# Optimization experiments

Measured on AMD Instinct MI355X. Metric: run time of the kernel, lower is better.

The kernel has to match this reference:

```python
import jax, jax.numpy as jnp
import numpy as np

SR = 16000
N_WT = 10
WT_LEN = 512
FIR_TAPS = 31
NU_C = 0.1
N_REFLECT = (FIR_TAPS - 1) // 2
B, L = 16, 160000


def setup_inputs() -> dict:
    key = jax.random.key(0)
    k1, k2, k3, k4 = jax.random.split(key, 4)
    # F0 in a realistic [100, 400) Hz range
    pitch = jax.random.uniform(k1, (B, L, 1), jnp.float32) * 300.0 + 100.0
    envelope = jax.random.uniform(k2, (B, L, 1), jnp.float32)
    # attention weights are 'already softmaxed' over the wavetable axis
    attention = jax.nn.softmax(jax.random.normal(k3, (B, L, N_WT), jnp.float32), axis=-1)
    # learned wavetables, init N(0, 0.01) as in the torch module (n_pure_harmonics=0)
    wavetables = jax.random.normal(k4, (N_WT, WT_LEN), jnp.float32) * 0.01
    # fixed windowed-sinc low-pass FIR (Type I), same construction as __init__
    n = np.arange(-(FIR_TAPS - 1) // 2, 1 + (FIR_TAPS - 1) // 2, dtype=np.float32)
    h = 2.0 * NU_C * np.sinc(2.0 * NU_C * n) * np.hamming(FIR_TAPS)
    fir_h = jnp.asarray(h, jnp.float32)
    return {"pitch": pitch, "envelope": envelope, "attention": attention,
            "wavetables": wavetables, "fir_h": fir_h}


def reference(pitch, envelope, attention, wavetables, fir_h):
    # circular ('reflect' in the repo's naming) pad each wavetable: (W, 512+2*15)
    wt_pad = jnp.concatenate(
        [wavetables[:, -N_REFLECT:], wavetables, wavetables[:, :N_REFLECT]], axis=1)
    # torch conv1d is cross-correlation; jnp.correlate 'valid' matches -> (W, 512)
    wt = jax.vmap(lambda x: jnp.correlate(x, fir_h, mode='valid'))(wt_pad)

    L_wt = WT_LEN
    freqs = pitch[..., 0]                       # (B, L)
    increment = (L_wt / SR) * freqs             # phase increment per sample
    # NOTE: faithful to torch code: increment[0] is the FIRST BATCH ROW (L,)
    index = jnp.cumsum(increment, axis=1) - increment[0]
    index = jnp.remainder(index, L_wt)
    index = jnp.where(L_wt - index < 1e-5, 0.0, index)
    idx_lo_f = jnp.floor(index)
    alpha = index - idx_lo_f                    # (B, L)
    i_lo = idx_lo_f.astype(jnp.int32)
    i_hi = jnp.ceil(index).astype(jnp.int32) % L_wt

    # gather all wavetables at once: (W, B, L)
    lo = jnp.take(wt, i_lo, axis=1)
    hi = jnp.take(wt, i_hi, axis=1)
    wave = lo + alpha[None, :, :] * (hi - lo)   # linear interpolation
    wave = jnp.transpose(wave, (1, 2, 0))       # (B, L, W)

    out = jnp.sum(wave * attention, axis=2, keepdims=True) * envelope  # (B, L, 1)
    return out
```

## Files before the change

### kernel.cpp

```cpp
#include <hip/hip_runtime.h>

#define N_WT_     10
#define WT_LEN_   512
#define FIR_TAPS_ 31
#define N_REFL_   15
#define B_        16
#define L_        160000

constexpr int   TPB   = 256;
constexpr float INCF  = 0.032f;
constexpr int   NG0   = L_ / 16;
constexpr int   NG1   = NG0 / 16;
constexpr int   NG2   = 40;
constexpr int   NG3   = 3;
constexpr int   CPB   = 5;
constexpr int   WTI   = (WT_LEN_ + 1) * N_WT_;

__global__ void fir_kernel(const float* __restrict__ wavetables,
                           const float* __restrict__ fir_h,
                           float* __restrict__ wt2) {
    __shared__ float s_pad[WT_LEN_ + 2 * N_REFL_];
    __shared__ float s_h[FIR_TAPS_];
    const int w = blockIdx.x;
    const int i = threadIdx.x;
    if (i < FIR_TAPS_) s_h[i] = fir_h[i];
    for (int j = i; j < WT_LEN_ + 2 * N_REFL_; j += blockDim.x) {
        int src = (j + WT_LEN_ - N_REFL_) % WT_LEN_;
        s_pad[j] = wavetables[w * WT_LEN_ + src];
    }
    __syncthreads();
    float acc = 0.0f;
#pragma unroll
    for (int t = 0; t < FIR_TAPS_; ++t)
        acc = fmaf(s_h[t], s_pad[i + t], acc);
    wt2[i * N_WT_ + w] = acc;
    if (i == 0) wt2[WT_LEN_ * N_WT_ + w] = acc;
}

__global__ __launch_bounds__(TPB) void ysum_kernel(
        const float* __restrict__ pitch, float* __restrict__ y) {
    __shared__ float s_x[4096];
    const int b = blockIdx.y, bx = blockIdx.x, t = threadIdx.x;
    const float* prow = pitch + (size_t)b * L_;
    const int x0 = bx * 4096;
    for (int i = t; i < 4096; i += TPB) {
        int l = x0 + i;
        s_x[i] = (l < L_) ? INCF * prow[l] : 0.0f;
    }
    __syncthreads();
    const int g = bx * 256 + t;
    if (g < NG0) {
        const float* p = s_x + (g * 16 - x0);
        float acc = 0.0f;
        for (int i = 0; i < 16; ++i) acc += p[i];
        y[b * NG0 + g] = acc;
    }
}

__global__ __launch_bounds__(TPB) void scan_kernel(
        const float* __restrict__ y, float* __restrict__ S1) {
    __shared__ float s_y[NG0];
    __shared__ float s_S1[NG0];
    __shared__ float s_z[NG1];
    __shared__ float s_S2[NG1];
    __shared__ float s_w[NG2], s_S3[NG2];
    __shared__ float s_v[NG3], s_S4[NG3];
    const int b = blockIdx.x, t = threadIdx.x;
    const float* yrow = y + (size_t)b * NG0;
    for (int i = t; i < NG0; i += TPB) s_y[i] = yrow[i];
    __syncthreads();
    for (int j = t; j < NG1; j += TPB) {
        float a = 0.0f;
        for (int i = 0; i < 16; ++i) a += s_y[16 * j + i];
        s_z[j] = a;
    }
    __syncthreads();
    if (t < NG2) {
        float a = 0.0f;
        int hi = min(16 * t + 16, NG1);
        for (int i = 16 * t; i < hi; ++i) a += s_z[i];
        s_w[t] = a;
    }
    __syncthreads();
    if (t < NG3) {
        float a = 0.0f;
        int hi = min(16 * t + 16, NG2);
        for (int i = 16 * t; i < hi; ++i) a += s_w[i];
        s_v[t] = a;
    }
    __syncthreads();
    if (t == 0) {
        float run = 0.0f;
        for (int m = 0; m < NG3; ++m) { run += s_v[m]; s_S4[m] = run; }
    }
    __syncthreads();
    if (t < NG2) {
        float a = 0.0f;
        for (int i = (t >> 4) << 4; i <= t; ++i) a += s_w[i];
        if (t >= 16) a = a + s_S4[(t >> 4) - 1];
        s_S3[t] = a;
    }
    __syncthreads();
    if (t < NG2) {
        float r = 0.0f;
        float carry = (t > 0) ? s_S3[t - 1] : 0.0f;
        int hi = min(16 * t + 16, NG1);
        for (int k = 16 * t; k < hi; ++k) {
            r += s_z[k];
            s_S2[k] = (t > 0) ? r + carry : r;
        }
    }
    __syncthreads();
    for (int j = t; j < NG1; j += TPB) {
        float r = 0.0f;
        float carry = (j > 0) ? s_S2[j - 1] : 0.0f;
        for (int k = 0; k < 16; ++k) {
            r += s_y[16 * j + k];
            s_S1[16 * j + k] = (j > 0) ? r + carry : r;
        }
    }
    __syncthreads();
    float* S1row = S1 + (size_t)b * NG0;
    for (int i = t; i < NG0; i += TPB) S1row[i] = s_S1[i];
}

__global__ __launch_bounds__(TPB) void synth_kernel(
        const float* __restrict__ pitch,
        const float* __restrict__ envelope,
        const float* __restrict__ attention,
        const float* __restrict__ wt2,
        const float* __restrict__ S1,
        float* __restrict__ out) {
    __shared__ float s_wt[WTI];
    const int b = blockIdx.y, cb = blockIdx.x, t = threadIdx.x;
    for (int i = t; i < WTI; i += TPB) s_wt[i] = wt2[i];
    __syncthreads();

    const int lane = t & 63;
    const int r16  = lane & 15;
    const int sbase = lane & ~15;
    const size_t rowb = (size_t)b * L_;
    const float* S1row = S1 + (size_t)b * NG0;

    for (int cc = 0; cc < CPB; ++cc) {
        const int    l = (cb * CPB + cc) * TPB + t;
        const size_t g = rowb + l;

        float x = INCF * pitch[g];
        float acc = 0.0f;
#pragma unroll
        for (int k = 0; k < 16; ++k) {
            float v = __shfl(x, sbase + k, 64);
            acc += (k <= r16) ? v : 0.0f;
        }
        const int g0 = l >> 4;
        if (g0 > 0) acc = acc + S1row[g0 - 1];

        float idx = acc - INCF * pitch[l];
        float r = fmodf(idx, 512.0f);
        if (r < 0.0f) r += 512.0f;
        if (512.0f - r < 1e-5f) r = 0.0f;
        float fl = floorf(r);
        float alpha = r - fl;
        int lo = (int)fl;

        const float2* pw = (const float2*)(s_wt + lo * N_WT_);
        float2 q0 = pw[0], q1 = pw[1], q2 = pw[2], q3 = pw[3], q4 = pw[4];
        float2 q5 = pw[5], q6 = pw[6], q7 = pw[7], q8 = pw[8], q9 = pw[9];
        float loV[10] = {q0.x, q0.y, q1.x, q1.y, q2.x, q2.y, q3.x, q3.y, q4.x, q4.y};
        float hiV[10] = {q5.x, q5.y, q6.x, q6.y, q7.x, q7.y, q8.x, q8.y, q9.x, q9.y};

        const float2* ap = (const float2*)(attention + g * N_WT_);
        float2 a01 = ap[0], a23 = ap[1], a45 = ap[2], a67 = ap[3], a89 = ap[4];
        float a[10] = {a01.x, a01.y, a23.x, a23.y, a45.x, a45.y,
                       a67.x, a67.y, a89.x, a89.y};

        float a0 = 0.0f;
#pragma unroll
        for (int w = 0; w < N_WT_; ++w)
            a0 += a[w] * (loV[w] + alpha * (hiV[w] - loV[w]));
        out[g] = a0 * envelope[g];
    }
}

extern "C" void kernel_launch(void* const* d_in, const int* in_sizes, int n_in,
                              void* d_out, int out_size, void* d_ws, size_t ws_size,
                              hipStream_t stream) {
    const float* pitch      = (const float*)d_in[0];
    const float* envelope   = (const float*)d_in[1];
    const float* attention  = (const float*)d_in[2];
    const float* wavetables = (const float*)d_in[3];
    const float* fir_h      = (const float*)d_in[4];
    float*       out        = (float*)d_out;

    char*  ws  = (char*)d_ws;
    float* wt2 = (float*)(ws);
    float* y   = (float*)(ws + 32768);
    float* S1  = (float*)(ws + 32768 + 655360);

    fir_kernel<<<dim3(N_WT_), dim3(WT_LEN_), 0, stream>>>(wavetables, fir_h, wt2);
    ysum_kernel<<<dim3(40, B_), dim3(TPB), 0, stream>>>(pitch, y);
    scan_kernel<<<dim3(B_), dim3(TPB), 0, stream>>>(y, S1);
    synth_kernel<<<dim3(L_ / (TPB * CPB), B_), dim3(TPB), 0, stream>>>(
        pitch, envelope, attention, wt2, S1, out);
}
```

Baseline: 203.2 us.

## Fuse FIR into ysum, widen scan block, one chunk per synth block

The FIR wavetable filter moves into the first ten blocks of the ysum kernel, which removes one kernel launch. The scan kernel runs with 1024 threads and copies rows with float2 loads and stores. The synth kernel now handles one 256-element chunk per block and has many more blocks. Its global loads (pitch, envelope, attention, carry) are issued before the shared wavetable fill so they overlap it. In exchange, each synth block reloads the whole shared wavetable for less work, and the fused blocks carry extra FIR work and shared memory.

```diff
diff --git a/kernel.cpp b/kernel.cpp
--- a/kernel.cpp
+++ b/kernel.cpp
@@ -8,39 +8,32 @@
 #define L_        160000
 
 constexpr int   TPB   = 256;
+constexpr int   TPS   = 1024;
 constexpr float INCF  = 0.032f;
 constexpr int   NG0   = L_ / 16;
 constexpr int   NG1   = NG0 / 16;
 constexpr int   NG2   = 40;
 constexpr int   NG3   = 3;
-constexpr int   CPB   = 5;
 constexpr int   WTI   = (WT_LEN_ + 1) * N_WT_;
 
-__global__ void fir_kernel(const float* __restrict__ wavetables,
-                           const float* __restrict__ fir_h,
-                           float* __restrict__ wt2) {
+__global__ __launch_bounds__(TPB) void ysum_kernel(
+        const float* __restrict__ pitch, float* __restrict__ y,
+        const float* __restrict__ wavetables, const float* __restrict__ fir_h,
+        float* __restrict__ wt2) {
+    __shared__ float s_x[4096];
     __shared__ float s_pad[WT_LEN_ + 2 * N_REFL_];
     __shared__ float s_h[FIR_TAPS_];
-    const int w = blockIdx.x;
-    const int i = threadIdx.x;
-    if (i < FIR_TAPS_) s_h[i] = fir_h[i];
-    for (int j = i; j < WT_LEN_ + 2 * N_REFL_; j += blockDim.x) {
-        int src = (j + WT_LEN_ - N_REFL_) % WT_LEN_;
-        s_pad[j] = wavetables[w * WT_LEN_ + src];
-    }
-    __syncthreads();
-    float acc = 0.0f;
-#pragma unroll
-    for (int t = 0; t < FIR_TAPS_; ++t)
-        acc = fmaf(s_h[t], s_pad[i + t], acc);
-    wt2[i * N_WT_ + w] = acc;
-    if (i == 0) wt2[WT_LEN_ * N_WT_ + w] = acc;
-}
-
-__global__ __launch_bounds__(TPB) void ysum_kernel(
-        const float* __restrict__ pitch, float* __restrict__ y) {
-    __shared__ float s_x[4096];
     const int b = blockIdx.y, bx = blockIdx.x, t = threadIdx.x;
+
+    const bool do_fir = (b == 0) && (bx < N_WT_);
+    if (do_fir) {
+        if (t < FIR_TAPS_) s_h[t] = fir_h[t];
+        for (int j = t; j < WT_LEN_ + 2 * N_REFL_; j += TPB) {
+            int src = (j + WT_LEN_ - N_REFL_) % WT_LEN_;
+            s_pad[j] = wavetables[bx * WT_LEN_ + src];
+        }
+    }
+
     const float* prow = pitch + (size_t)b * L_;
     const int x0 = bx * 4096;
     for (int i = t; i < 4096; i += TPB) {
@@ -48,6 +41,18 @@
         s_x[i] = (l < L_) ? INCF * prow[l] : 0.0f;
     }
     __syncthreads();
+
+    if (do_fir) {
+        for (int i = t; i < WT_LEN_; i += TPB) {
+            float acc = 0.0f;
+#pragma unroll
+            for (int tap = 0; tap < FIR_TAPS_; ++tap)
+                acc = fmaf(s_h[tap], s_pad[i + tap], acc);
+            wt2[i * N_WT_ + bx] = acc;
+            if (i == 0) wt2[WT_LEN_ * N_WT_ + bx] = acc;
+        }
+    }
+
     const int g = bx * 256 + t;
     if (g < NG0) {
         const float* p = s_x + (g * 16 - x0);
@@ -57,19 +62,23 @@
     }
 }
 
-__global__ __launch_bounds__(TPB) void scan_kernel(
+__global__ __launch_bounds__(TPS) void scan_kernel(
         const float* __restrict__ y, float* __restrict__ S1) {
-    __shared__ float s_y[NG0];
-    __shared__ float s_S1[NG0];
+    __shared__ __align__(16) float s_y[NG0];
+    __shared__ __align__(16) float s_S1[NG0];
     __shared__ float s_z[NG1];
     __shared__ float s_S2[NG1];
     __shared__ float s_w[NG2], s_S3[NG2];
     __shared__ float s_v[NG3], s_S4[NG3];
     const int b = blockIdx.x, t = threadIdx.x;
     const float* yrow = y + (size_t)b * NG0;
-    for (int i = t; i < NG0; i += TPB) s_y[i] = yrow[i];
-    __syncthreads();
-    for (int j = t; j < NG1; j += TPB) {
+    {
+        const float2* src = (const float2*)yrow;
+        float2* dst = (float2*)s_y;
+        for (int i = t; i < NG0 / 2; i += TPS) dst[i] = src[i];
+    }
+    __syncthreads();
+    for (int j = t; j < NG1; j += TPS) {
         float a = 0.0f;
         for (int i = 0; i < 16; ++i) a += s_y[16 * j + i];
         s_z[j] = a;
@@ -111,7 +120,7 @@
         }
     }
     __syncthreads();
-    for (int j = t; j < NG1; j += TPB) {
+    for (int j = t; j < NG1; j += TPS) {
         float r = 0.0f;
         float carry = (j > 0) ? s_S2[j - 1] : 0.0f;
         for (int k = 0; k < 16; ++k) {
@@ -121,7 +130,11 @@
     }
     __syncthreads();
     float* S1row = S1 + (size_t)b * NG0;
-    for (int i = t; i < NG0; i += TPB) S1row[i] = s_S1[i];
+    {
+        const float2* src = (const float2*)s_S1;
+        float2* dst = (float2*)S1row;
+        for (int i = t; i < NG0 / 2; i += TPS) dst[i] = src[i];
+    }
 }
 
 __global__ __launch_bounds__(TPB) void synth_kernel(
@@ -131,56 +144,60 @@
         const float* __restrict__ wt2,
         const float* __restrict__ S1,
         float* __restrict__ out) {
-    __shared__ float s_wt[WTI];
+    __shared__ __align__(16) float s_wt[WTI];
     const int b = blockIdx.y, cb = blockIdx.x, t = threadIdx.x;
-    for (int i = t; i < WTI; i += TPB) s_wt[i] = wt2[i];
-    __syncthreads();
-
-    const int lane = t & 63;
-    const int r16  = lane & 15;
+    const int    l = cb * TPB + t;
+    const size_t g = (size_t)b * L_ + l;
+
+    const float pv  = pitch[g];
+    const float p0  = pitch[l];
+    const float env = envelope[g];
+    const int   g0  = l >> 4;
+    const float carry = (g0 > 0) ? S1[(size_t)b * NG0 + g0 - 1] : 0.0f;
+    const float2* ap = (const float2*)(attention + g * (size_t)N_WT_);
+    float2 a01 = ap[0], a23 = ap[1], a45 = ap[2], a67 = ap[3], a89 = ap[4];
+
+    {
+        const float2* src = (const float2*)wt2;
+        float2* dst = (float2*)s_wt;
+        for (int i = t; i < WTI / 2; i += TPB) dst[i] = src[i];
+    }
+    __syncthreads();
+
+    const int lane  = t & 63;
+    const int r16   = lane & 15;
     const int sbase = lane & ~15;
-    const size_t rowb = (size_t)b * L_;
-    const float* S1row = S1 + (size_t)b * NG0;
-
-    for (int cc = 0; cc < CPB; ++cc) {
-        const int    l = (cb * CPB + cc) * TPB + t;
-        const size_t g = rowb + l;
-
-        float x = INCF * pitch[g];
-        float acc = 0.0f;
+
+    float x = INCF * pv;
+    float acc = 0.0f;
 #pragma unroll
-        for (int k = 0; k < 16; ++k) {
-            float v = __shfl(x, sbase + k, 64);
-            acc += (k <= r16) ? v : 0.0f;
-        }
-        const int g0 = l >> 4;
-        if (g0 > 0) acc = acc + S1row[g0 - 1];
-
-        float idx = acc - INCF * pitch[l];
-        float r = fmodf(idx, 512.0f);
-        if (r < 0.0f) r += 512.0f;
-        if (512.0f - r < 1e-5f) r = 0.0f;
-        float fl = floorf(r);
-        float alpha = r - fl;
-        int lo = (int)fl;
-
-        const float2* pw = (const float2*)(s_wt + lo * N_WT_);
-        float2 q0 = pw[0], q1 = pw[1], q2 = pw[2], q3 = pw[3], q4 = pw[4];
-        float2 q5 = pw[5], q6 = pw[6], q7 = pw[7], q8 = pw[8], q9 = pw[9];
-        float loV[10] = {q0.x, q0.y, q1.x, q1.y, q2.x, q2.y, q3.x, q3.y, q4.x, q4.y};
-        float hiV[10] = {q5.x, q5.y, q6.x, q6.y, q7.x, q7.y, q8.x, q8.y, q9.x, q9.y};
-
-        const float2* ap = (const float2*)(attention + g * N_WT_);
-        float2 a01 = ap[0], a23 = ap[1], a45 = ap[2], a67 = ap[3], a89 = ap[4];
-        float a[10] = {a01.x, a01.y, a23.x, a23.y, a45.x, a45.y,
-                       a67.x, a67.y, a89.x, a89.y};
-
-        float a0 = 0.0f;
+    for (int k = 0; k < 16; ++k) {
+        float v = __shfl(x, sbase + k, 64);
+        acc += (k <= r16) ? v : 0.0f;
+    }
+    if (g0 > 0) acc = acc + carry;
+
+    float idx = acc - INCF * p0;
+    float r = fmodf(idx, 512.0f);
+    if (r < 0.0f) r += 512.0f;
+    if (512.0f - r < 1e-5f) r = 0.0f;
+    float fl = floorf(r);
+    float alpha = r - fl;
+    int lo = (int)fl;
+
+    const float2* pw = (const float2*)(s_wt + lo * N_WT_);
+    float2 q0 = pw[0], q1 = pw[1], q2 = pw[2], q3 = pw[3], q4 = pw[4];
+    float2 q5 = pw[5], q6 = pw[6], q7 = pw[7], q8 = pw[8], q9 = pw[9];
+    float loV[10] = {q0.x, q0.y, q1.x, q1.y, q2.x, q2.y, q3.x, q3.y, q4.x, q4.y};
+    float hiV[10] = {q5.x, q5.y, q6.x, q6.y, q7.x, q7.y, q8.x, q8.y, q9.x, q9.y};
+    float a[10] = {a01.x, a01.y, a23.x, a23.y, a45.x, a45.y,
+                   a67.x, a67.y, a89.x, a89.y};
+
+    float a0 = 0.0f;
 #pragma unroll
-        for (int w = 0; w < N_WT_; ++w)
-            a0 += a[w] * (loV[w] + alpha * (hiV[w] - loV[w]));
-        out[g] = a0 * envelope[g];
-    }
+    for (int w = 0; w < N_WT_; ++w)
+        a0 += a[w] * (loV[w] + alpha * (hiV[w] - loV[w]));
+    out[g] = a0 * env;
 }
 
 extern "C" void kernel_launch(void* const* d_in, const int* in_sizes, int n_in,
@@ -198,9 +215,9 @@
     float* y   = (float*)(ws + 32768);
     float* S1  = (float*)(ws + 32768 + 655360);
 
-    fir_kernel<<<dim3(N_WT_), dim3(WT_LEN_), 0, stream>>>(wavetables, fir_h, wt2);
-    ysum_kernel<<<dim3(40, B_), dim3(TPB), 0, stream>>>(pitch, y);
-    scan_kernel<<<dim3(B_), dim3(TPB), 0, stream>>>(y, S1);
-    synth_kernel<<<dim3(L_ / (TPB * CPB), B_), dim3(TPB), 0, stream>>>(
+    ysum_kernel<<<dim3(40, B_), dim3(TPB), 0, stream>>>(
+        pitch, y, wavetables, fir_h, wt2);
+    scan_kernel<<<dim3(B_), dim3(TPS), 0, stream>>>(y, S1);
+    synth_kernel<<<dim3(NG1, B_), dim3(TPB), 0, stream>>>(
         pitch, envelope, attention, wt2, S1, out);
 }
```

Result: no change. 201.4 us (-0.9%).
